# Kernel tuning notes

Hardware: AMD Instinct MI355X
Metric: run time of the kernel (lower is better)

## Reference

```python
import jax, jax.numpy as jnp
import numpy as np

SEQ, BATCH, NFEAT, HID = 512, 128, 64, 256


def setup_inputs() -> dict:
    key = jax.random.key(0)
    ks = jax.random.split(key, 11)
    s = 0.05
    return {
        "X": jax.random.normal(ks[0], (SEQ, BATCH, NFEAT), jnp.float32),
        "w_ih0": jax.random.normal(ks[1], (4 * HID, NFEAT), jnp.float32) * s,
        "w_hh0": jax.random.normal(ks[2], (4 * HID, HID), jnp.float32) * s,
        "b_ih0": jax.random.normal(ks[3], (4 * HID,), jnp.float32) * s,
        "b_hh0": jax.random.normal(ks[4], (4 * HID,), jnp.float32) * s,
        "w_ih1": jax.random.normal(ks[5], (4 * HID, HID), jnp.float32) * s,
        "w_hh1": jax.random.normal(ks[6], (4 * HID, HID), jnp.float32) * s,
        "b_ih1": jax.random.normal(ks[7], (4 * HID,), jnp.float32) * s,
        "b_hh1": jax.random.normal(ks[8], (4 * HID,), jnp.float32) * s,
        "fc_w": jax.random.normal(ks[9], (1, HID), jnp.float32) * s,
        "fc_b": jax.random.normal(ks[10], (1,), jnp.float32) * s,
    }


def _lstm_layer(x, w_ih, w_hh, b_ih, b_hh):
    # x: [S, B, F]; PyTorch gate order: i, f, g, o along the 4H axis.
    S, B, _ = x.shape
    H = w_hh.shape[1]
    # Precompute input projection for all timesteps (batched GEMM).
    xp = jnp.einsum("sbf,gf->sbg", x, w_ih) + b_ih + b_hh  # [S, B, 4H]
    w_hh_t = w_hh.T  # [H, 4H]

    def step(carry, xt):
        h, c = carry
        gates = xt + h @ w_hh_t  # [B, 4H]
        i, f, g, o = jnp.split(gates, 4, axis=-1)
        i = jax.nn.sigmoid(i)
        f = jax.nn.sigmoid(f)
        g = jnp.tanh(g)
        o = jax.nn.sigmoid(o)
        c = f * c + i * g
        h = o * jnp.tanh(c)
        return (h, c), h

    h0 = jnp.zeros((B, H), x.dtype)
    c0 = jnp.zeros((B, H), x.dtype)
    _, out = jax.lax.scan(step, (h0, c0), xp)
    return out  # [S, B, H]


def reference(X, w_ih0, w_hh0, b_ih0, b_hh0, w_ih1, w_hh1, b_ih1, b_hh1, fc_w, fc_b):
    out0 = _lstm_layer(X, w_ih0, w_hh0, b_ih0, b_hh0)
    out1 = _lstm_layer(out0, w_ih1, w_hh1, b_ih1, b_hh1)
    last = out1[-1]  # [B, H]
    return last @ fc_w.T + fc_b  # [B, 1]
```

## Files before the change

kernel.cpp:

```cpp
#include <hip/hip_runtime.h>

#define SEQ   512
#define BATCH 128
#define NFEAT 64
#define HID   256
#define HB    (BATCH * HID)
#define NGRP  8
#define GBLK  32


typedef unsigned u32;
typedef unsigned long long u64;
typedef __attribute__((ext_vector_type(8))) short  short8;
typedef __attribute__((ext_vector_type(4))) float  f32x4;
typedef __attribute__((ext_vector_type(4))) unsigned short us4;

__device__ __forceinline__ unsigned short f2bf(float f) {
    union { float f; unsigned u; } c; c.f = f;
    unsigned r = c.u + 0x7FFF + ((c.u >> 16) & 1);
    return (unsigned short)(r >> 16);
}
__device__ __forceinline__ float bf2f(unsigned short h) {
    union { float f; unsigned u; } c; c.u = ((unsigned)h) << 16;
    return c.f;
}

__device__ __forceinline__ u64 ald64(const u64* p) {
    return __hip_atomic_load(p, __ATOMIC_RELAXED, __HIP_MEMORY_SCOPE_AGENT);
}
__device__ __forceinline__ u32 ald32(const u32* p) {
    return __hip_atomic_load(p, __ATOMIC_RELAXED, __HIP_MEMORY_SCOPE_AGENT);
}
__device__ __forceinline__ void ast32(u32* p, u32 v) {
    __hip_atomic_store(p, v, __ATOMIC_RELAXED, __HIP_MEMORY_SCOPE_AGENT);
}
__device__ __forceinline__ void agld16(const u32* p, u32 w[16]) {
    const u64* q = (const u64*)p;
    #pragma unroll
    for (int i = 0; i < 8; ++i) {
        const u64 v = ald64(q + i);
        w[2 * i] = (u32)v; w[2 * i + 1] = (u32)(v >> 32);
    }
}

__global__ __launch_bounds__(256, 1) void lstm_persist(
    const float* __restrict__ X,
    const float* __restrict__ w_ih0,
    const float* __restrict__ w_hh0,
    const float* __restrict__ b_ih0,
    const float* __restrict__ b_hh0,
    const float* __restrict__ w_ih1,
    const float* __restrict__ w_hh1,
    const float* __restrict__ b_ih1,
    const float* __restrict__ b_hh1,
    u32* __restrict__ h0p,
    u32* __restrict__ h1p,
    u32* __restrict__ flags)
{
    const int bid = blockIdx.x;
    const int tid = threadIdx.x;
    const int g     = bid >> 5;
    const int rk    = bid & 31;
    const int layer = rk >> 4;
    const int ct    = rk & 15;
    const int b0    = g * 16;
    const int j0    = ct * 16;

    const int wave = tid >> 6;
    const int l    = tid & 63;
    const int kq   = l >> 4;
    const int ar   = l & 15;

    __shared__ __align__(16) unsigned short hsh[16 * 512];
    __shared__ __align__(16) unsigned short hsl[16 * 512];
    __shared__ float red[4][4][16][20];
    __shared__ float bbuf[4][16];

    {
        const short8 z8 = {0, 0, 0, 0, 0, 0, 0, 0};
        for (int i = tid; i < 16 * 512 / 8; i += 256) {
            ((short8*)hsh)[i] = z8;
            ((short8*)hsl)[i] = z8;
        }
    }
    if (tid < 64) {
        const int gg = tid >> 4, cc = tid & 15;
        const float* bi_ = layer ? b_ih1 : b_ih0;
        const float* bh_ = layer ? b_hh1 : b_hh0;
        bbuf[gg][cc] = bi_[gg * 256 + j0 + cc] + bh_[gg * 256 + j0 + cc];
    }

    short8 Ahi[4][4], Alo[4][4];
    {
        const short8 z8 = {0, 0, 0, 0, 0, 0, 0, 0};
        #pragma unroll
        for (int gg = 0; gg < 4; ++gg) {
            const int row = gg * 256 + j0 + ar;
            #pragma unroll
            for (int kt = 0; kt < 4; ++kt) {
                const int k = (wave * 4 + kt) * 32 + kq * 8;
                const float* src = nullptr;
                if (layer) {
                    src = (k < 256) ? (w_ih1 + (size_t)row * 256 + k)
                                    : (w_hh1 + (size_t)row * 256 + (k - 256));
                } else {
                    if (k < 64)       src = w_ih0 + (size_t)row * 64 + k;
                    else if (k < 320) src = w_hh0 + (size_t)row * 256 + (k - 64);
                }
                short8 hi8 = z8, lo8 = z8;
                if (src) {
                    const float4 a = ((const float4*)src)[0];
                    const float4 b = ((const float4*)src)[1];
                    const float wv[8] = {a.x, a.y, a.z, a.w, b.x, b.y, b.z, b.w};
                    #pragma unroll
                    for (int i = 0; i < 8; ++i) {
                        const unsigned short h = f2bf(wv[i]);
                        hi8[i] = (short)h;
                        lo8[i] = (short)f2bf(wv[i] - bf2f(h));
                    }
                }
                Ahi[gg][kt] = hi8;
                Alo[gg][kt] = lo8;
            }
        }
    }

    const int eb = tid >> 4, ecc = tid & 15;
    float creg = 0.f;

    u32* hown  = layer ? h1p : h0p;
    u32* gflag = flags + (size_t)g * GBLK * 32;
    const int hoff = layer ? 256 : 64;

    const int pb = tid >> 4, pf = tid & 15;
    float4 xpf = make_float4(0.f, 0.f, 0.f, 0.f);
    if (!layer)
        xpf = ((const float4*)(X + (size_t)(b0 + pb) * NFEAT))[pf];

    __syncthreads();

    for (int t = 0; t < SEQ; ++t) {
        const int sp  = (t - 1) & 3;
        const int st  = t & 3;
        const u32 tgp = (t > 0) ? ((u32)((t - 1) >> 2) % 3u) + 1u : 0u;
        const u32 tgc = ((u32)(t >> 2) % 3u) + 1u;

        const u32* faddr = nullptr;
        u32 fthr = 0, fval = 0;
        if (tid < 16) {
            if (tid != ct && t >= 3) {
                faddr = &gflag[(layer * 16 + tid) * 32];
                fthr  = (u32)(t - 2);
            }
        } else if (tid < 32 && layer == 0 && t >= 4) {
            faddr = &gflag[(16 + (tid - 16)) * 32];
            fthr  = (u32)(t - 3);
        }
        if (faddr) fval = ald32(faddr);

        const int b = tid >> 4, f0 = tid & 15;
        const int swz = (b & 7) << 3;

        if (t > 0) {
            const u32* hp = hown + (size_t)sp * HB + (size_t)(b0 + b) * HID + f0 * 16;
            u32 w[16];
            int guard = 0;
            for (;;) {
                agld16(hp, w);
                bool ok = true;
                #pragma unroll
                for (int i = 0; i < 16; ++i) ok &= ((w[i] & 3u) == tgp);
                if (ok || ++guard >= (1 << 14)) break;
            }
            short8 h0v, l0v, h1v, l1v;
            #pragma unroll
            for (int i = 0; i < 8; ++i) {
                h0v[i] = (short)(w[i] >> 16);     l0v[i] = (short)(w[i] & 0xFFFCu);
                h1v[i] = (short)(w[8 + i] >> 16); l1v[i] = (short)(w[8 + i] & 0xFFFCu);
            }
            const int us = b * 512 + hoff + f0 * 16;
            *(short8*)&hsh[us ^ swz]       = h0v;
            *(short8*)&hsh[(us + 8) ^ swz] = h1v;
            *(short8*)&hsl[us ^ swz]       = l0v;
            *(short8*)&hsl[(us + 8) ^ swz] = l1v;
        }
        if (layer) {
            const u32* xp = h0p + (size_t)st * HB + (size_t)(b0 + b) * HID + f0 * 16;
            u32 w[16];
            int guard = 0;
            for (;;) {
                agld16(xp, w);
                bool ok = true;
                #pragma unroll
                for (int i = 0; i < 16; ++i) ok &= ((w[i] & 3u) == tgc);
                if (ok || ++guard >= (1 << 14)) break;
            }
            short8 h0v, l0v, h1v, l1v;
            #pragma unroll
            for (int i = 0; i < 8; ++i) {
                h0v[i] = (short)(w[i] >> 16);     l0v[i] = (short)(w[i] & 0xFFFCu);
                h1v[i] = (short)(w[8 + i] >> 16); l1v[i] = (short)(w[8 + i] & 0xFFFCu);
            }
            const int us = b * 512 + f0 * 16;
            *(short8*)&hsh[us ^ swz]       = h0v;
            *(short8*)&hsh[(us + 8) ^ swz] = h1v;
            *(short8*)&hsl[us ^ swz]       = l0v;
            *(short8*)&hsl[(us + 8) ^ swz] = l1v;
        } else {
            const float xv[4] = {xpf.x, xpf.y, xpf.z, xpf.w};
            us4 xh, xl;
            #pragma unroll
            for (int i = 0; i < 4; ++i) {
                const unsigned short hh = f2bf(xv[i]);
                xh[i] = hh;
                xl[i] = (unsigned short)(f2bf(xv[i] - bf2f(hh)) & 0xFFFF);
            }
            const int us = pb * 512 + pf * 4;
            const int sw = (pb & 7) << 3;
            *(us4*)&hsh[us ^ sw] = xh;
            *(us4*)&hsl[us ^ sw] = xl;
        }

        if (faddr) {
            int guard = 0;
            while (fval < fthr && ++guard < (1 << 16)) fval = ald32(faddr);
        }
        __syncthreads();

        if (tid == 0)
            ast32(&gflag[rk * 32], (u32)(t + 1));

        if (!layer && t + 1 < SEQ)
            xpf = ((const float4*)(X + (size_t)(t + 1) * BATCH * NFEAT
                                     + (size_t)(b0 + pb) * NFEAT))[pf];

        {
            f32x4 acc[4];
            #pragma unroll
            for (int gg = 0; gg < 4; ++gg)
                acc[gg] = (f32x4){0.f, 0.f, 0.f, 0.f};

            #pragma unroll
            for (int kt = 0; kt < 4; ++kt) {
                const int KT = wave * 4 + kt;
                const int us = ar * 512 + KT * 32 + kq * 8;
                const int uswz = us ^ ((ar & 7) << 3);
                const short8 bh = *(const short8*)&hsh[uswz];
                const short8 bl = *(const short8*)&hsl[uswz];
                #pragma unroll
                for (int gg = 0; gg < 4; ++gg)
                    acc[gg] = __builtin_amdgcn_mfma_f32_16x16x32_bf16(
                        Ahi[gg][kt], bh, acc[gg], 0, 0, 0);
                #pragma unroll
                for (int gg = 0; gg < 4; ++gg)
                    acc[gg] = __builtin_amdgcn_mfma_f32_16x16x32_bf16(
                        Alo[gg][kt], bh, acc[gg], 0, 0, 0);
                #pragma unroll
                for (int gg = 0; gg < 4; ++gg)
                    acc[gg] = __builtin_amdgcn_mfma_f32_16x16x32_bf16(
                        Ahi[gg][kt], bl, acc[gg], 0, 0, 0);
            }
            #pragma unroll
            for (int gg = 0; gg < 4; ++gg)
                *(f32x4*)&red[wave][gg][ar][kq * 4] = acc[gg];
        }
        __syncthreads();

        {
            float p[4];
            #pragma unroll
            for (int gg = 0; gg < 4; ++gg)
                p[gg] = bbuf[gg][ecc] + red[0][gg][eb][ecc] + red[1][gg][eb][ecc]
                                      + red[2][gg][eb][ecc] + red[3][gg][eb][ecc];
            const float ig  = 1.0f / (1.0f + __expf(-p[0]));
            const float fg  = 1.0f / (1.0f + __expf(-p[1]));
            const float gg_ = tanhf(p[2]);
            const float og  = 1.0f / (1.0f + __expf(-p[3]));
            creg = fg * creg + ig * gg_;
            const float hv = og * tanhf(creg);
            const unsigned short hi = f2bf(hv);
            const unsigned short lo = f2bf(hv - bf2f(hi));
            ast32(&hown[(size_t)st * HB + (size_t)(b0 + eb) * HID + j0 + ecc],
                  ((u32)hi << 16) | ((u32)lo & 0xFFFCu) | tgc);
        }
    }
}

__global__ __launch_bounds__(64) void fc_kernel(
    const u32* __restrict__ h1last_p,
    const float* __restrict__ fc_w,
    const float* __restrict__ fc_b,
    float* __restrict__ out)
{
    const int b    = blockIdx.x;
    const int lane = threadIdx.x;
    float sum = 0.0f;
    #pragma unroll
    for (int k = lane; k < HID; k += 64) {
        const u32 w = h1last_p[(size_t)b * HID + k];
        const float h = bf2f((unsigned short)(w >> 16))
                      + bf2f((unsigned short)(w & 0xFFFCu));
        sum += h * fc_w[k];
    }
    #pragma unroll
    for (int off = 32; off > 0; off >>= 1)
        sum += __shfl_down(sum, off);
    if (lane == 0) out[b] = sum + fc_b[0];
}

extern "C" void kernel_launch(void* const* d_in, const int* in_sizes, int n_in,
                              void* d_out, int out_size, void* d_ws, size_t ws_size,
                              hipStream_t stream)
{
    const float* X     = (const float*)d_in[0];
    const float* w_ih0 = (const float*)d_in[1];
    const float* w_hh0 = (const float*)d_in[2];
    const float* b_ih0 = (const float*)d_in[3];
    const float* b_hh0 = (const float*)d_in[4];
    const float* w_ih1 = (const float*)d_in[5];
    const float* w_hh1 = (const float*)d_in[6];
    const float* b_ih1 = (const float*)d_in[7];
    const float* b_hh1 = (const float*)d_in[8];
    const float* fc_w  = (const float*)d_in[9];
    const float* fc_b  = (const float*)d_in[10];

    u32* h0p   = (u32*)d_ws;
    u32* h1p   = h0p + 4 * HB;
    u32* flags = h1p + 4 * HB;

    const size_t zbytes = (size_t)(8 * HB + NGRP * GBLK * 32) * sizeof(u32);
    (void)hipMemsetAsync(d_ws, 0, zbytes, stream);

    lstm_persist<<<NGRP * GBLK, 256, 0, stream>>>(X,
        w_ih0, w_hh0, b_ih0, b_hh0,
        w_ih1, w_hh1, b_ih1, b_hh1,
        h0p, h1p, flags);

    fc_kernel<<<BATCH, 64, 0, stream>>>(h1p + 3 * HB, fc_w, fc_b, (float*)d_out);
}
```

Before: 2.199 ms.

## Interleave two 8-row batch sets per block to overlap polling with compute

Each block now handles two independent 8-batch-row sets (A and B) instead of one 16-row group. The step alternates front/back phases between the sets, and the global loads for one set are issued while the other set computes. The aim is to hide the cross-block h-state polling latency behind useful work. The trade-off is a new set-major workspace layout, separate flags per set, and MFMA tiles that are half empty per set, since only 8 of the 16 rows are valid.

```diff
diff --git a/kernel.cpp b/kernel.cpp
--- a/kernel.cpp
+++ b/kernel.cpp
@@ -5,8 +5,9 @@
 #define NFEAT 64
 #define HID   256
 #define HB    (BATCH * HID)
-#define NGRP  8
+#define NPAIR 8
 #define GBLK  32
+#define SETW  2048
 
 
 typedef unsigned u32;
@@ -40,6 +41,16 @@
     for (int i = 0; i < 8; ++i) {
         const u64 v = ald64(q + i);
         w[2 * i] = (u32)v; w[2 * i + 1] = (u32)(v >> 32);
+    }
+}
+__device__ __forceinline__ void spin16(const u32* p, u32 w[16], u32 tag) {
+    int guard = 0;
+    for (;;) {
+        bool ok = true;
+        #pragma unroll
+        for (int i = 0; i < 16; ++i) ok &= ((w[i] & 3u) == tag);
+        if (ok || ++guard >= (1 << 14)) break;
+        agld16(p, w);
     }
 }
 
@@ -59,17 +70,22 @@
 {
     const int bid = blockIdx.x;
     const int tid = threadIdx.x;
-    const int g     = bid >> 5;
+    const int p     = bid >> 5;
     const int rk    = bid & 31;
     const int layer = rk >> 4;
     const int ct    = rk & 15;
-    const int b0    = g * 16;
     const int j0    = ct * 16;
+    const int setA  = 2 * p, setB = 2 * p + 1;
 
     const int wave = tid >> 6;
     const int l    = tid & 63;
     const int kq   = l >> 4;
     const int ar   = l & 15;
+
+    const int b  = tid >> 5;
+    const int f0 = tid & 31;
+    const int pbloc = (tid & 127) >> 4;
+    const int pf    = tid & 15;
 
     __shared__ __align__(16) unsigned short hsh[16 * 512];
     __shared__ __align__(16) unsigned short hsl[16 * 512];
@@ -110,8 +126,8 @@
                 short8 hi8 = z8, lo8 = z8;
                 if (src) {
                     const float4 a = ((const float4*)src)[0];
-                    const float4 b = ((const float4*)src)[1];
-                    const float wv[8] = {a.x, a.y, a.z, a.w, b.x, b.y, b.z, b.w};
+                    const float4 bq = ((const float4*)src)[1];
+                    const float wv[8] = {a.x, a.y, a.z, a.w, bq.x, bq.y, bq.z, bq.w};
                     #pragma unroll
                     for (int i = 0; i < 8; ++i) {
                         const unsigned short h = f2bf(wv[i]);
@@ -126,87 +142,65 @@
     }
 
     const int eb = tid >> 4, ecc = tid & 15;
-    float creg = 0.f;
-
-    u32* hown  = layer ? h1p : h0p;
-    u32* gflag = flags + (size_t)g * GBLK * 32;
+    float cregA = 0.f, cregB = 0.f;
+    u32 wA[16], wB[16];
+
+    u32* hown = layer ? h1p : h0p;
     const int hoff = layer ? 256 : 64;
 
-    const int pb = tid >> 4, pf = tid & 15;
-    float4 xpf = make_float4(0.f, 0.f, 0.f, 0.f);
-    if (!layer)
-        xpf = ((const float4*)(X + (size_t)(b0 + pb) * NFEAT))[pf];
-
-    __syncthreads();
-
-    for (int t = 0; t < SEQ; ++t) {
-        const int sp  = (t - 1) & 3;
-        const int st  = t & 3;
+    auto issue = [&](int t, int set, u32* w) {
+        if (t >= SEQ) return;
+        if (t > 0 && f0 < 16)
+            agld16(hown + ((size_t)(((t - 1) & 3) * 16 + set)) * SETW
+                        + b * 256 + f0 * 16, w);
+        else if (layer && f0 >= 16)
+            agld16(h0p + ((size_t)((t & 3) * 16 + set)) * SETW
+                       + b * 256 + (f0 - 16) * 16, w);
+    };
+    auto unpack_to = [&](const u32* w, int us, int sw) {
+        short8 h0v, l0v, h1v, l1v;
+        #pragma unroll
+        for (int i = 0; i < 8; ++i) {
+            h0v[i] = (short)(w[i] >> 16);     l0v[i] = (short)(w[i] & 0xFFFCu);
+            h1v[i] = (short)(w[8 + i] >> 16); l1v[i] = (short)(w[8 + i] & 0xFFFCu);
+        }
+        *(short8*)&hsh[us ^ sw]       = h0v;
+        *(short8*)&hsh[(us + 8) ^ sw] = h1v;
+        *(short8*)&hsl[us ^ sw]       = l0v;
+        *(short8*)&hsl[(us + 8) ^ sw] = l1v;
+    };
+
+    auto front = [&](int t, int set, u32* w, float4& xpf, bool xmine, int fb) {
+        const int sp = (t - 1) & 3, st = t & 3;
         const u32 tgp = (t > 0) ? ((u32)((t - 1) >> 2) % 3u) + 1u : 0u;
         const u32 tgc = ((u32)(t >> 2) % 3u) + 1u;
-
-        const u32* faddr = nullptr;
-        u32 fthr = 0, fval = 0;
+        const int sw = b << 3;
+
+        const u32* faddr = nullptr; u32 fthr = 0, fval = 0;
         if (tid < 16) {
             if (tid != ct && t >= 3) {
-                faddr = &gflag[(layer * 16 + tid) * 32];
+                faddr = &flags[(size_t)(fb + layer * 16 + tid) * 32];
                 fthr  = (u32)(t - 2);
             }
         } else if (tid < 32 && layer == 0 && t >= 4) {
-            faddr = &gflag[(16 + (tid - 16)) * 32];
+            faddr = &flags[(size_t)(fb + 16 + (tid - 16)) * 32];
             fthr  = (u32)(t - 3);
         }
         if (faddr) fval = ald32(faddr);
 
-        const int b = tid >> 4, f0 = tid & 15;
-        const int swz = (b & 7) << 3;
-
-        if (t > 0) {
-            const u32* hp = hown + (size_t)sp * HB + (size_t)(b0 + b) * HID + f0 * 16;
-            u32 w[16];
-            int guard = 0;
-            for (;;) {
-                agld16(hp, w);
-                bool ok = true;
-                #pragma unroll
-                for (int i = 0; i < 16; ++i) ok &= ((w[i] & 3u) == tgp);
-                if (ok || ++guard >= (1 << 14)) break;
-            }
-            short8 h0v, l0v, h1v, l1v;
-            #pragma unroll
-            for (int i = 0; i < 8; ++i) {
-                h0v[i] = (short)(w[i] >> 16);     l0v[i] = (short)(w[i] & 0xFFFCu);
-                h1v[i] = (short)(w[8 + i] >> 16); l1v[i] = (short)(w[8 + i] & 0xFFFCu);
-            }
-            const int us = b * 512 + hoff + f0 * 16;
-            *(short8*)&hsh[us ^ swz]       = h0v;
-            *(short8*)&hsh[(us + 8) ^ swz] = h1v;
-            *(short8*)&hsl[us ^ swz]       = l0v;
-            *(short8*)&hsl[(us + 8) ^ swz] = l1v;
+        if (t > 0 && f0 < 16) {
+            const u32* hp = hown + ((size_t)(sp * 16 + set)) * SETW + b * 256 + f0 * 16;
+            spin16(hp, w, tgp);
+            unpack_to(w, b * 512 + hoff + f0 * 16, sw);
         }
         if (layer) {
-            const u32* xp = h0p + (size_t)st * HB + (size_t)(b0 + b) * HID + f0 * 16;
-            u32 w[16];
-            int guard = 0;
-            for (;;) {
-                agld16(xp, w);
-                bool ok = true;
-                #pragma unroll
-                for (int i = 0; i < 16; ++i) ok &= ((w[i] & 3u) == tgc);
-                if (ok || ++guard >= (1 << 14)) break;
-            }
-            short8 h0v, l0v, h1v, l1v;
-            #pragma unroll
-            for (int i = 0; i < 8; ++i) {
-                h0v[i] = (short)(w[i] >> 16);     l0v[i] = (short)(w[i] & 0xFFFCu);
-                h1v[i] = (short)(w[8 + i] >> 16); l1v[i] = (short)(w[8 + i] & 0xFFFCu);
-            }
-            const int us = b * 512 + f0 * 16;
-            *(short8*)&hsh[us ^ swz]       = h0v;
-            *(short8*)&hsh[(us + 8) ^ swz] = h1v;
-            *(short8*)&hsl[us ^ swz]       = l0v;
-            *(short8*)&hsl[(us + 8) ^ swz] = l1v;
-        } else {
+            if (f0 >= 16) {
+                const u32* xp = h0p + ((size_t)(st * 16 + set)) * SETW
+                                    + b * 256 + (f0 - 16) * 16;
+                spin16(xp, w, tgc);
+                unpack_to(w, b * 512 + (f0 - 16) * 16, sw);
+            }
+        } else if (xmine) {
             const float xv[4] = {xpf.x, xpf.y, xpf.z, xpf.w};
             us4 xh, xl;
             #pragma unroll
@@ -215,12 +209,11 @@
                 xh[i] = hh;
                 xl[i] = (unsigned short)(f2bf(xv[i] - bf2f(hh)) & 0xFFFF);
             }
-            const int us = pb * 512 + pf * 4;
-            const int sw = (pb & 7) << 3;
-            *(us4*)&hsh[us ^ sw] = xh;
-            *(us4*)&hsl[us ^ sw] = xl;
-        }
-
+            const int us = pbloc * 512 + pf * 4;
+            const int sw2 = (pbloc & 7) << 3;
+            *(us4*)&hsh[us ^ sw2] = xh;
+            *(us4*)&hsl[us ^ sw2] = xl;
+        }
         if (faddr) {
             int guard = 0;
             while (fval < fthr && ++guard < (1 << 16)) fval = ald32(faddr);
@@ -228,18 +221,15 @@
         __syncthreads();
 
         if (tid == 0)
-            ast32(&gflag[rk * 32], (u32)(t + 1));
-
-        if (!layer && t + 1 < SEQ)
+            ast32(&flags[(size_t)(fb + rk) * 32], (u32)(t + 1));
+        if (!layer && xmine && t + 1 < SEQ)
             xpf = ((const float4*)(X + (size_t)(t + 1) * BATCH * NFEAT
-                                     + (size_t)(b0 + pb) * NFEAT))[pf];
+                                     + (size_t)(set * 8 + pbloc) * NFEAT))[pf];
 
         {
             f32x4 acc[4];
             #pragma unroll
-            for (int gg = 0; gg < 4; ++gg)
-                acc[gg] = (f32x4){0.f, 0.f, 0.f, 0.f};
-
+            for (int gg = 0; gg < 4; ++gg) acc[gg] = (f32x4){0.f, 0.f, 0.f, 0.f};
             #pragma unroll
             for (int kt = 0; kt < 4; ++kt) {
                 const int KT = wave * 4 + kt;
@@ -265,39 +255,69 @@
                 *(f32x4*)&red[wave][gg][ar][kq * 4] = acc[gg];
         }
         __syncthreads();
-
-        {
-            float p[4];
-            #pragma unroll
-            for (int gg = 0; gg < 4; ++gg)
-                p[gg] = bbuf[gg][ecc] + red[0][gg][eb][ecc] + red[1][gg][eb][ecc]
-                                      + red[2][gg][eb][ecc] + red[3][gg][eb][ecc];
-            const float ig  = 1.0f / (1.0f + __expf(-p[0]));
-            const float fg  = 1.0f / (1.0f + __expf(-p[1]));
-            const float gg_ = tanhf(p[2]);
-            const float og  = 1.0f / (1.0f + __expf(-p[3]));
-            creg = fg * creg + ig * gg_;
-            const float hv = og * tanhf(creg);
-            const unsigned short hi = f2bf(hv);
-            const unsigned short lo = f2bf(hv - bf2f(hi));
-            ast32(&hown[(size_t)st * HB + (size_t)(b0 + eb) * HID + j0 + ecc],
-                  ((u32)hi << 16) | ((u32)lo & 0xFFFCu) | tgc);
-        }
+    };
+
+    auto back = [&](int t, int set, float& creg) {
+        if (tid >= 128) return;
+        const int st = t & 3;
+        const u32 tgc = ((u32)(t >> 2) % 3u) + 1u;
+        float pr[4];
+        #pragma unroll
+        for (int gg = 0; gg < 4; ++gg)
+            pr[gg] = bbuf[gg][ecc] + red[0][gg][eb][ecc] + red[1][gg][eb][ecc]
+                                   + red[2][gg][eb][ecc] + red[3][gg][eb][ecc];
+        const float ig  = 1.0f / (1.0f + __expf(-pr[0]));
+        const float fg  = 1.0f / (1.0f + __expf(-pr[1]));
+        const float gg_ = tanhf(pr[2]);
+        const float og  = 1.0f / (1.0f + __expf(-pr[3]));
+        creg = fg * creg + ig * gg_;
+        const float hv = og * tanhf(creg);
+        const unsigned short hi = f2bf(hv);
+        const unsigned short lo = f2bf(hv - bf2f(hi));
+        ast32(&hown[((size_t)(st * 16 + set)) * SETW + eb * 256 + j0 + ecc],
+              ((u32)hi << 16) | ((u32)lo & 0xFFFCu) | tgc);
+    };
+
+    float4 xpfA = make_float4(0.f, 0.f, 0.f, 0.f);
+    float4 xpfB = make_float4(0.f, 0.f, 0.f, 0.f);
+    if (!layer) {
+        if (tid < 128)
+            xpfA = ((const float4*)(X + (size_t)(setA * 8 + pbloc) * NFEAT))[pf];
+        else
+            xpfB = ((const float4*)(X + (size_t)(setB * 8 + pbloc) * NFEAT))[pf];
+    }
+    const int fbA = 0 * NPAIR * GBLK + p * GBLK;
+    const int fbB = 1 * NPAIR * GBLK + p * GBLK;
+
+    __syncthreads();
+
+    issue(0, setA, wA);
+    issue(0, setB, wB);
+
+    for (int t = 0; t < SEQ; ++t) {
+        front(t, setA, wA, xpfA, tid < 128, fbA);
+        issue(t, setB, wB);
+        back(t, setA, cregA);
+        front(t, setB, wB, xpfB, tid >= 128, fbB);
+        issue(t + 1, setA, wA);
+        back(t, setB, cregB);
     }
 }
 
 __global__ __launch_bounds__(64) void fc_kernel(
-    const u32* __restrict__ h1last_p,
+    const u32* __restrict__ h1p,
     const float* __restrict__ fc_w,
     const float* __restrict__ fc_b,
     float* __restrict__ out)
 {
-    const int b    = blockIdx.x;
+    const int bg   = blockIdx.x;
     const int lane = threadIdx.x;
+    const int set = bg >> 3, bb = bg & 7;
+    const u32* row = h1p + ((size_t)(3 * 16 + set)) * SETW + bb * 256;
     float sum = 0.0f;
     #pragma unroll
     for (int k = lane; k < HID; k += 64) {
-        const u32 w = h1last_p[(size_t)b * HID + k];
+        const u32 w = row[k];
         const float h = bf2f((unsigned short)(w >> 16))
                       + bf2f((unsigned short)(w & 0xFFFCu));
         sum += h * fc_w[k];
@@ -305,7 +325,7 @@
     #pragma unroll
     for (int off = 32; off > 0; off >>= 1)
         sum += __shfl_down(sum, off);
-    if (lane == 0) out[b] = sum + fc_b[0];
+    if (lane == 0) out[bg] = sum + fc_b[0];
 }
 
 extern "C" void kernel_launch(void* const* d_in, const int* in_sizes, int n_in,
@@ -328,13 +348,14 @@
     u32* h1p   = h0p + 4 * HB;
     u32* flags = h1p + 4 * HB;
 
-    const size_t zbytes = (size_t)(8 * HB + NGRP * GBLK * 32) * sizeof(u32);
+    const size_t zbytes =
+        (size_t)(8 * HB + 2 * NPAIR * GBLK * 32) * sizeof(u32);
     (void)hipMemsetAsync(d_ws, 0, zbytes, stream);
 
-    lstm_persist<<<NGRP * GBLK, 256, 0, stream>>>(X,
+    lstm_persist<<<NPAIR * GBLK, 256, 0, stream>>>(X,
         w_ih0, w_hh0, b_ih0, b_hh0,
         w_ih1, w_hh1, b_ih1, b_hh1,
         h0p, h1p, flags);
 
-    fc_kernel<<<BATCH, 64, 0, stream>>>(h1p + 3 * HB, fc_w, fc_b, (float*)d_out);
-}
+    fc_kernel<<<BATCH, 64, 0, stream>>>(h1p, fc_w, fc_b, (float*)d_out);
+}
```

Result: slower. 2.944 ms (+33.9%).

## Split gate rows across waves to drop cross-wave LDS reduction

Applied to the files above, without the earlier changes.

Each wave now owns 4 output columns for all four gates over the full K dimension, instead of splitting K across waves. This removes the shared-memory partial-sum buffer and one barrier, and replaces them with two lane shuffles that regroup the gate values per thread. Layer 0 skips the all-zero K tiles (10 instead of 16). In exchange, each wave runs a longer serial MFMA chain per step and holds 16 A-fragments per wave in registers.

```diff
diff --git a/kernel.cpp b/kernel.cpp
--- a/kernel.cpp
+++ b/kernel.cpp
@@ -40,6 +40,17 @@
     for (int i = 0; i < 8; ++i) {
         const u64 v = ald64(q + i);
         w[2 * i] = (u32)v; w[2 * i + 1] = (u32)(v >> 32);
+    }
+}
+__device__ __forceinline__ void spin16(const u32* p, u32 w[16], u32 tag) {
+    int guard = 0;
+    agld16(p, w);
+    for (;;) {
+        bool ok = true;
+        #pragma unroll
+        for (int i = 0; i < 16; ++i) ok &= ((w[i] & 3u) == tag);
+        if (ok || ++guard >= (1 << 14)) break;
+        agld16(p, w);
     }
 }
 
@@ -73,7 +84,6 @@
 
     __shared__ __align__(16) unsigned short hsh[16 * 512];
     __shared__ __align__(16) unsigned short hsl[16 * 512];
-    __shared__ float red[4][4][16][20];
     __shared__ float bbuf[4][16];
 
     {
@@ -90,42 +100,41 @@
         bbuf[gg][cc] = bi_[gg * 256 + j0 + cc] + bh_[gg * 256 + j0 + cc];
     }
 
-    short8 Ahi[4][4], Alo[4][4];
+    short8 Ahi[16], Alo[16];
     {
         const short8 z8 = {0, 0, 0, 0, 0, 0, 0, 0};
+        const int gate = ar >> 2, coff = ar & 3;
+        const int row  = gate * 256 + j0 + wave * 4 + coff;
         #pragma unroll
-        for (int gg = 0; gg < 4; ++gg) {
-            const int row = gg * 256 + j0 + ar;
-            #pragma unroll
-            for (int kt = 0; kt < 4; ++kt) {
-                const int k = (wave * 4 + kt) * 32 + kq * 8;
-                const float* src = nullptr;
-                if (layer) {
-                    src = (k < 256) ? (w_ih1 + (size_t)row * 256 + k)
-                                    : (w_hh1 + (size_t)row * 256 + (k - 256));
-                } else {
-                    if (k < 64)       src = w_ih0 + (size_t)row * 64 + k;
-                    else if (k < 320) src = w_hh0 + (size_t)row * 256 + (k - 64);
+        for (int KT = 0; KT < 16; ++KT) {
+            const int k = KT * 32 + kq * 8;
+            const float* src = nullptr;
+            if (layer) {
+                src = (k < 256) ? (w_ih1 + (size_t)row * 256 + k)
+                                : (w_hh1 + (size_t)row * 256 + (k - 256));
+            } else {
+                if (k < 64)       src = w_ih0 + (size_t)row * 64 + k;
+                else if (k < 320) src = w_hh0 + (size_t)row * 256 + (k - 64);
+            }
+            short8 hi8 = z8, lo8 = z8;
+            if (src) {
+                const float4 a = ((const float4*)src)[0];
+                const float4 bq = ((const float4*)src)[1];
+                const float wv[8] = {a.x, a.y, a.z, a.w, bq.x, bq.y, bq.z, bq.w};
+                #pragma unroll
+                for (int i = 0; i < 8; ++i) {
+                    const unsigned short h = f2bf(wv[i]);
+                    hi8[i] = (short)h;
+                    lo8[i] = (short)f2bf(wv[i] - bf2f(h));
                 }
-                short8 hi8 = z8, lo8 = z8;
-                if (src) {
-                    const float4 a = ((const float4*)src)[0];
-                    const float4 b = ((const float4*)src)[1];
-                    const float wv[8] = {a.x, a.y, a.z, a.w, b.x, b.y, b.z, b.w};
-                    #pragma unroll
-                    for (int i = 0; i < 8; ++i) {
-                        const unsigned short h = f2bf(wv[i]);
-                        hi8[i] = (short)h;
-                        lo8[i] = (short)f2bf(wv[i] - bf2f(h));
-                    }
-                }
-                Ahi[gg][kt] = hi8;
-                Alo[gg][kt] = lo8;
-            }
-        }
-    }
-
-    const int eb = tid >> 4, ecc = tid & 15;
+            }
+            Ahi[KT] = hi8;
+            Alo[KT] = lo8;
+        }
+    }
+    const int KTMAX = layer ? 16 : 10;
+
+    const int oq = l >> 4, ob = l & 15;
     float creg = 0.f;
 
     u32* hown  = layer ? h1p : h0p;
@@ -145,8 +154,7 @@
         const u32 tgp = (t > 0) ? ((u32)((t - 1) >> 2) % 3u) + 1u : 0u;
         const u32 tgc = ((u32)(t >> 2) % 3u) + 1u;
 
-        const u32* faddr = nullptr;
-        u32 fthr = 0, fval = 0;
+        const u32* faddr = nullptr; u32 fthr = 0, fval = 0;
         if (tid < 16) {
             if (tid != ct && t >= 3) {
                 faddr = &gflag[(layer * 16 + tid) * 32];
@@ -164,14 +172,7 @@
         if (t > 0) {
             const u32* hp = hown + (size_t)sp * HB + (size_t)(b0 + b) * HID + f0 * 16;
             u32 w[16];
-            int guard = 0;
-            for (;;) {
-                agld16(hp, w);
-                bool ok = true;
-                #pragma unroll
-                for (int i = 0; i < 16; ++i) ok &= ((w[i] & 3u) == tgp);
-                if (ok || ++guard >= (1 << 14)) break;
-            }
+            spin16(hp, w, tgp);
             short8 h0v, l0v, h1v, l1v;
             #pragma unroll
             for (int i = 0; i < 8; ++i) {
@@ -187,14 +188,7 @@
         if (layer) {
             const u32* xp = h0p + (size_t)st * HB + (size_t)(b0 + b) * HID + f0 * 16;
             u32 w[16];
-            int guard = 0;
-            for (;;) {
-                agld16(xp, w);
-                bool ok = true;
-                #pragma unroll
-                for (int i = 0; i < 16; ++i) ok &= ((w[i] & 3u) == tgc);
-                if (ok || ++guard >= (1 << 14)) break;
-            }
+            spin16(xp, w, tgc);
             short8 h0v, l0v, h1v, l1v;
             #pragma unroll
             for (int i = 0; i < 8; ++i) {
@@ -234,55 +228,58 @@
             xpf = ((const float4*)(X + (size_t)(t + 1) * BATCH * NFEAT
                                      + (size_t)(b0 + pb) * NFEAT))[pf];
 
+        f32x4 aHH = (f32x4){0.f, 0.f, 0.f, 0.f};
+        f32x4 aHL = (f32x4){0.f, 0.f, 0.f, 0.f};
+        f32x4 aLH = (f32x4){0.f, 0.f, 0.f, 0.f};
+        for (int KT = 0; KT < KTMAX; ++KT) {
+            const int us = ar * 512 + KT * 32 + kq * 8;
+            const int uswz = us ^ ((ar & 7) << 3);
+            const short8 bh = *(const short8*)&hsh[uswz];
+            const short8 bl = *(const short8*)&hsl[uswz];
+            aHH = __builtin_amdgcn_mfma_f32_16x16x32_bf16(Ahi[KT], bh, aHH, 0, 0, 0);
+            aHL = __builtin_amdgcn_mfma_f32_16x16x32_bf16(Ahi[KT], bl, aHL, 0, 0, 0);
+            aLH = __builtin_amdgcn_mfma_f32_16x16x32_bf16(Alo[KT], bh, aLH, 0, 0, 0);
+        }
+        float v0 = aHH[0] + aHL[0] + aLH[0];
+        float v1 = aHH[1] + aHL[1] + aLH[1];
+        float v2 = aHH[2] + aHL[2] + aLH[2];
+        float v3 = aHH[3] + aHL[3] + aLH[3];
+
         {
-            f32x4 acc[4];
-            #pragma unroll
-            for (int gg = 0; gg < 4; ++gg)
-                acc[gg] = (f32x4){0.f, 0.f, 0.f, 0.f};
-
-            #pragma unroll
-            for (int kt = 0; kt < 4; ++kt) {
-                const int KT = wave * 4 + kt;
-                const int us = ar * 512 + KT * 32 + kq * 8;
-                const int uswz = us ^ ((ar & 7) << 3);
-                const short8 bh = *(const short8*)&hsh[uswz];
-                const short8 bl = *(const short8*)&hsl[uswz];
-                #pragma unroll
-                for (int gg = 0; gg < 4; ++gg)
-                    acc[gg] = __builtin_amdgcn_mfma_f32_16x16x32_bf16(
-                        Ahi[gg][kt], bh, acc[gg], 0, 0, 0);
-                #pragma unroll
-                for (int gg = 0; gg < 4; ++gg)
-                    acc[gg] = __builtin_amdgcn_mfma_f32_16x16x32_bf16(
-                        Alo[gg][kt], bh, acc[gg], 0, 0, 0);
-                #pragma unroll
-                for (int gg = 0; gg < 4; ++gg)
-                    acc[gg] = __builtin_amdgcn_mfma_f32_16x16x32_bf16(
-                        Ahi[gg][kt], bl, acc[gg], 0, 0, 0);
-            }
-            #pragma unroll
-            for (int gg = 0; gg < 4; ++gg)
-                *(f32x4*)&red[wave][gg][ar][kq * 4] = acc[gg];
-        }
-        __syncthreads();
-
+            const bool hi = (l >> 4) & 1;
+            float s0 = hi ? v0 : v1;
+            float s1 = hi ? v2 : v3;
+            const float r0 = __shfl_xor(s0, 16);
+            const float r1 = __shfl_xor(s1, 16);
+            if (hi) { v0 = r0; v2 = r1; } else { v1 = r0; v3 = r1; }
+        }
         {
-            float p[4];
-            #pragma unroll
-            for (int gg = 0; gg < 4; ++gg)
-                p[gg] = bbuf[gg][ecc] + red[0][gg][eb][ecc] + red[1][gg][eb][ecc]
-                                      + red[2][gg][eb][ecc] + red[3][gg][eb][ecc];
-            const float ig  = 1.0f / (1.0f + __expf(-p[0]));
-            const float fg  = 1.0f / (1.0f + __expf(-p[1]));
-            const float gg_ = tanhf(p[2]);
-            const float og  = 1.0f / (1.0f + __expf(-p[3]));
+            const bool hi = (l >> 5) & 1;
+            float s0 = hi ? v0 : v2;
+            float s1 = hi ? v1 : v3;
+            const float r0 = __shfl_xor(s0, 32);
+            const float r1 = __shfl_xor(s1, 32);
+            if (hi) { v0 = r0; v1 = r1; } else { v2 = r0; v3 = r1; }
+        }
+
+        {
+            const int colq = wave * 4 + oq;
+            const float pi  = v0 + bbuf[0][colq];
+            const float pf_ = v1 + bbuf[1][colq];
+            const float pg  = v2 + bbuf[2][colq];
+            const float po  = v3 + bbuf[3][colq];
+            const float ig  = 1.0f / (1.0f + __expf(-pi));
+            const float fg  = 1.0f / (1.0f + __expf(-pf_));
+            const float gg_ = tanhf(pg);
+            const float og  = 1.0f / (1.0f + __expf(-po));
             creg = fg * creg + ig * gg_;
             const float hv = og * tanhf(creg);
             const unsigned short hi = f2bf(hv);
             const unsigned short lo = f2bf(hv - bf2f(hi));
-            ast32(&hown[(size_t)st * HB + (size_t)(b0 + eb) * HID + j0 + ecc],
+            ast32(&hown[(size_t)st * HB + (size_t)(b0 + ob) * HID + j0 + colq],
                   ((u32)hi << 16) | ((u32)lo & 0xFFFCu) | tgc);
         }
+        __syncthreads();
     }
 }
 
```

Result: slower. 4.217 ms (+91.8%).
